# Kernel optimization log

Hardware: AMD Instinct MI355X
Metric: run time of the kernel (lower is better)

The kernel has to match this reference:

```python
import jax, jax.numpy as jnp
import numpy as np

D_MODEL = 1024
N_HEADS = 16
HEAD_DIM = D_MODEL // N_HEADS


def setup_inputs() -> dict:
    key = jax.random.key(0)
    ks = jax.random.split(key, 5)
    T, B = 2048, 2
    x = jax.random.normal(ks[0], (T, B, D_MODEL), dtype=jnp.float32)
    s = 1.0 / np.sqrt(D_MODEL)
    Wq = jax.random.normal(ks[1], (D_MODEL, D_MODEL), dtype=jnp.float32) * s
    Wk = jax.random.normal(ks[2], (D_MODEL, D_MODEL), dtype=jnp.float32) * s
    Wv = jax.random.normal(ks[3], (D_MODEL, D_MODEL), dtype=jnp.float32) * s
    Wo = jax.random.normal(ks[4], (D_MODEL, D_MODEL), dtype=jnp.float32) * s
    return {"x": x, "Wq": Wq, "Wk": Wk, "Wv": Wv, "Wo": Wo}


def reference(x, Wq, Wk, Wv, Wo):
    T, B, C = x.shape
    H, D = N_HEADS, HEAD_DIM

    def split_heads(t):
        # (T,B,C) -> (B,H,T,D), matching view+permute(1,2,0,3)
        return t.reshape(T, B, H, D).transpose(1, 2, 0, 3)

    q = split_heads(x @ Wq.T)
    k = split_heads(x @ Wk.T)
    v = split_heads(x @ Wv.T)

    scale = 1.0 / jnp.sqrt(jnp.asarray(D, dtype=x.dtype))
    scores = jnp.einsum('bhqd,bhkd->bhqk', q, k) * scale  # (B,H,T,T)
    causal = jnp.tril(jnp.ones((T, T), dtype=bool))
    scores = jnp.where(causal, scores, jnp.asarray(-jnp.inf, dtype=scores.dtype))
    probs = jax.nn.softmax(scores, axis=-1)
    ctx = jnp.einsum('bhqk,bhkd->bhqd', probs, v)  # (B,H,T,D)
    ctx = ctx.transpose(2, 0, 1, 3).reshape(T, B, C)
    return ctx @ Wo.T
```

## Files before the change

### kernel.cpp

```cpp
#include <hip/hip_runtime.h>
#include <hip/hip_bf16.h>

#define TT 2048
#define BB 2
#define CC 1024
#define HH 16
#define DD 64
#define MM (TT * BB)

typedef short bf16x8 __attribute__((ext_vector_type(8)));
typedef float f32x4  __attribute__((ext_vector_type(4)));

__device__ inline ushort f2b(float f) {
    union { float f; unsigned u; } v; v.f = f;
    unsigned r = v.u + 0x7FFFu + ((v.u >> 16) & 1u);
    return (ushort)(r >> 16);
}

__device__ inline unsigned pack_bf16(float a, float b) {
    __hip_bfloat162 h = __float22bfloat162_rn(make_float2(a, b));
    union { __hip_bfloat162 h; unsigned u; } c; c.h = h;
    return c.u;
}

__device__ inline void gload_lds16(const ushort* g, ushort* l) {
    __builtin_amdgcn_global_load_lds(
        (const __attribute__((address_space(1))) void*)g,
        (__attribute__((address_space(3))) void*)l, 16, 0, 0);
}

#define XQUADS (MM * CC / 4)
#define WQUADS (CC * CC / 4)
__global__ __launch_bounds__(256) void conv_all(const float* __restrict__ x,
                                                const float* __restrict__ Wq,
                                                const float* __restrict__ Wk,
                                                const float* __restrict__ Wv,
                                                const float* __restrict__ Wo,
                                                ushort* __restrict__ dst) {
    int idx = blockIdx.x * 256 + threadIdx.x;
    const float* src;
    int off;
    if (idx < XQUADS) {
        src = x; off = idx;
    } else {
        int wi = (idx - XQUADS) >> 18;
        off = (idx - XQUADS) & (WQUADS - 1);
        src = (wi == 0) ? Wq : (wi == 1) ? Wk : (wi == 2) ? Wv : Wo;
    }
    float4 v = ((const float4*)src)[off];
    ushort4 o = {f2b(v.x), f2b(v.y), f2b(v.z), f2b(v.w)};
    ((ushort4*)dst)[idx] = o;
}

__global__ __launch_bounds__(256) void gemm_qkv(const ushort* __restrict__ A,
                                                const ushort* __restrict__ B0,
                                                const ushort* __restrict__ B1,
                                                const ushort* __restrict__ B2,
                                                ushort* __restrict__ Oq,
                                                ushort* __restrict__ Ok,
                                                ushort* __restrict__ Ov) {
    __shared__ __align__(16) ushort As[128 * 32];
    __shared__ __align__(16) ushort Bs[128 * 32];

    const int tid = threadIdx.x;
    const int wave = tid >> 6, lane = tid & 63;
    const int quad = lane >> 4, l16 = lane & 15;
    const int wm = wave >> 1, wn = wave & 1;

    const int bm = blockIdx.x * 128;
    const int by = blockIdx.y;
    const int wsel = by >> 3;
    const ushort* Bp = (wsel == 0) ? B0 : (wsel == 1) ? B1 : B2;
    const int bn = (by & 7) * 128;

    const int srow = lane >> 2;
    const int scol = (lane & 3) * 8;

    f32x4 acc[4][4];
#pragma unroll
    for (int i = 0; i < 4; i++)
#pragma unroll
        for (int j = 0; j < 4; j++) acc[i][j] = (f32x4){0.f, 0.f, 0.f, 0.f};

    for (int k0 = 0; k0 < CC; k0 += 32) {
#pragma unroll
        for (int i = 0; i < 2; i++) {
            const int rbase = wave * 32 + i * 16;
            gload_lds16(A + (size_t)(bm + rbase + srow) * CC + k0 + scol,
                        As + rbase * 32);
            gload_lds16(Bp + (size_t)(bn + rbase + srow) * CC + k0 + scol,
                        Bs + rbase * 32);
        }
        __syncthreads();

        bf16x8 af[4], bf[4];
#pragma unroll
        for (int mi = 0; mi < 4; mi++)
            af[mi] = *(const bf16x8*)(As + (wm * 64 + mi * 16 + l16) * 32 + quad * 8);
#pragma unroll
        for (int ni = 0; ni < 4; ni++)
            bf[ni] = *(const bf16x8*)(Bs + (wn * 64 + ni * 16 + l16) * 32 + quad * 8);
#pragma unroll
        for (int mi = 0; mi < 4; mi++)
#pragma unroll
            for (int ni = 0; ni < 4; ni++)
                acc[mi][ni] = __builtin_amdgcn_mfma_f32_16x16x32_bf16(
                    af[mi], bf[ni], acc[mi][ni], 0, 0, 0);
        __syncthreads();
    }

#pragma unroll
    for (int mi = 0; mi < 4; mi++) {
#pragma unroll
        for (int r = 0; r < 4; r++) {
            const int m = bm + wm * 64 + mi * 16 + quad * 4 + r;
#pragma unroll
            for (int ni = 0; ni < 4; ni++) {
                const int colg = bn + wn * 64 + ni * 16 + l16;
                float v = acc[mi][ni][r];
                if (wsel == 0) v *= 0.18033688f;
                const int t = m >> 1, b = m & 1;
                const int h = colg >> 6, d = colg & 63;
                ushort* dst = (wsel == 0) ? Oq : (wsel == 1) ? Ok : Ov;
                dst[(((size_t)(b * HH + h)) * TT + t) * DD + d] = f2b(v);
            }
        }
    }
}

__global__ __launch_bounds__(256) void gemm_out(const ushort* __restrict__ A,
                                                const ushort* __restrict__ Bm,
                                                float* __restrict__ Of) {
    __shared__ __align__(16) ushort As[128 * 32];
    __shared__ __align__(16) ushort Bs[64 * 32];

    const int tid = threadIdx.x;
    const int wave = tid >> 6, lane = tid & 63;
    const int quad = lane >> 4, l16 = lane & 15;

    const int bm = blockIdx.x * 128;
    const int bn = blockIdx.y * 64;

    const int srow = lane >> 2;
    const int scol = (lane & 3) * 8;

    f32x4 acc[2][4];
#pragma unroll
    for (int i = 0; i < 2; i++)
#pragma unroll
        for (int j = 0; j < 4; j++) acc[i][j] = (f32x4){0.f, 0.f, 0.f, 0.f};

    for (int k0 = 0; k0 < CC; k0 += 32) {
#pragma unroll
        for (int i = 0; i < 2; i++) {
            const int rbase = wave * 32 + i * 16;
            gload_lds16(A + (size_t)(bm + rbase + srow) * CC + k0 + scol,
                        As + rbase * 32);
        }
        gload_lds16(Bm + (size_t)(bn + wave * 16 + srow) * CC + k0 + scol,
                    Bs + wave * 16 * 32);
        __syncthreads();

        bf16x8 af[2], bf[4];
#pragma unroll
        for (int mi = 0; mi < 2; mi++)
            af[mi] = *(const bf16x8*)(As + (wave * 32 + mi * 16 + l16) * 32 + quad * 8);
#pragma unroll
        for (int ni = 0; ni < 4; ni++)
            bf[ni] = *(const bf16x8*)(Bs + (ni * 16 + l16) * 32 + quad * 8);
#pragma unroll
        for (int mi = 0; mi < 2; mi++)
#pragma unroll
            for (int ni = 0; ni < 4; ni++)
                acc[mi][ni] = __builtin_amdgcn_mfma_f32_16x16x32_bf16(
                    af[mi], bf[ni], acc[mi][ni], 0, 0, 0);
        __syncthreads();
    }

#pragma unroll
    for (int mi = 0; mi < 2; mi++)
#pragma unroll
        for (int r = 0; r < 4; r++) {
            const int m = bm + wave * 32 + mi * 16 + quad * 4 + r;
#pragma unroll
            for (int ni = 0; ni < 4; ni++)
                Of[(size_t)m * CC + bn + ni * 16 + l16] = acc[mi][ni][r];
        }
}

__global__ __launch_bounds__(256) void prep_kv(const ushort* __restrict__ Kb,
                                               const ushort* __restrict__ Vb,
                                               ushort* __restrict__ Kf,
                                               ushort* __restrict__ Vf) {
    __shared__ __align__(16) ushort Ls[64 * 72];
    const int tile = blockIdx.x;
    const int bh   = blockIdx.y;
    const int t    = threadIdx.x;
    const size_t src = (size_t)bh * TT * DD + (size_t)tile * 64 * DD;
    const size_t dst = (size_t)bh * TT * DD + (size_t)tile * 4096;

#pragma unroll
    for (int i = 0; i < 2; i++) {
        int e = t + i * 256;
        int r = e >> 3, kc = (e & 7) * 8;
        *(uint4*)(Ls + r * 72 + kc) = *(const uint4*)(Kb + src + r * 64 + kc);
    }
    __syncthreads();
#pragma unroll
    for (int i = 0; i < 2; i++) {
        int o = t + i * 256;
        int c = o >> 8, nb = (o >> 6) & 3, lane = o & 63;
        int quad = lane >> 4, l16 = lane & 15;
        int j = nb * 16 + l16, k0 = c * 32 + quad * 8;
        *(uint4*)(Kf + dst + (size_t)o * 8) = *(const uint4*)(Ls + j * 72 + k0);
    }
    __syncthreads();

#pragma unroll
    for (int i = 0; i < 2; i++) {
        int e = t + i * 256;
        int r = e >> 3, kc = (e & 7) * 8;
        *(uint4*)(Ls + r * 72 + kc) = *(const uint4*)(Vb + src + r * 64 + kc);
    }
    __syncthreads();
#pragma unroll
    for (int i = 0; i < 2; i++) {
        int o = t + i * 256;
        int c = o >> 8, db = (o >> 6) & 3, lane = o & 63;
        int quad = lane >> 4, l16 = lane & 15;
        int d = db * 16 + l16;
        ushort tmp[8];
#pragma unroll
        for (int u = 0; u < 8; u++) {
            int jp = c * 32 + quad * 8 + u;
            int j = (jp & 3) * 16 + (jp >> 2);
            tmp[u] = Ls[j * 72 + d];
        }
        *(uint4*)(Vf + dst + (size_t)o * 8) = *(uint4*)tmp;
    }
}

template <bool DIAG>
__device__ __forceinline__ void attn_step(const bf16x8* qa, f32x4* O, float* l,
                                          const bf16x8* kf, const bf16x8* vf,
                                          ushort* P, int j0, int qbase,
                                          int quad, int l16) {
    f32x4 S[4];
#pragma unroll
    for (int nb = 0; nb < 4; nb++) S[nb] = (f32x4){0.f, 0.f, 0.f, 0.f};
#pragma unroll
    for (int c = 0; c < 2; c++)
#pragma unroll
        for (int nb = 0; nb < 4; nb++)
            S[nb] = __builtin_amdgcn_mfma_f32_16x16x32_bf16(qa[c], kf[c * 4 + nb],
                                                            S[nb], 0, 0, 0);

#pragma unroll
    for (int r = 0; r < 4; r++) {
        const int qg = qbase + quad * 4 + r;
        float p[4];
#pragma unroll
        for (int nb = 0; nb < 4; nb++) {
            float s = S[nb][r];
            if (DIAG) { if (j0 + nb * 16 + l16 > qg) s = -1e30f; }
            p[nb] = __builtin_amdgcn_exp2f(s);
        }
        l[r] += (p[0] + p[1]) + (p[2] + p[3]);
        uint2 w; w.x = pack_bf16(p[0], p[1]); w.y = pack_bf16(p[2], p[3]);
        *(uint2*)(P + (quad * 4 + r) * 72 + l16 * 4) = w;
    }

#pragma unroll
    for (int c = 0; c < 2; c++) {
        bf16x8 pa = *(const bf16x8*)(P + l16 * 72 + c * 32 + quad * 8);
#pragma unroll
        for (int db = 0; db < 4; db++)
            O[db] = __builtin_amdgcn_mfma_f32_16x16x32_bf16(pa, vf[c * 4 + db],
                                                            O[db], 0, 0, 0);
    }
}

__global__ __launch_bounds__(256, 2) void attn_mfma(const ushort* __restrict__ Qb,
                                                    const ushort* __restrict__ Kf,
                                                    const ushort* __restrict__ Vf,
                                                    ushort* __restrict__ ctx) {
    __shared__ __align__(16) ushort PsA[4 * 16 * 72];
    __shared__ __align__(16) ushort PsB[4 * 16 * 72];

    const int tid  = threadIdx.x;
    const int wave = tid >> 6;
    const int lane = tid & 63;
    const int quad = lane >> 4;
    const int l16  = lane & 15;

    const int p  = blockIdx.x;
    const int bh = blockIdx.y;
    const int qtA = p, qtB = (TT / 64 - 1) - p;
    const int q0A = qtA * 64 + wave * 16;
    const int q0B = qtB * 64 + wave * 16;

    const size_t baseQK = (size_t)bh * TT * DD;

    bf16x8 qaA[2], qaB[2];
    {
        const ushort* qp = Qb + baseQK + (size_t)(q0A + l16) * DD + quad * 8;
        qaA[0] = *(const bf16x8*)(qp);
        qaA[1] = *(const bf16x8*)(qp + 32);
        const ushort* qp2 = Qb + baseQK + (size_t)(q0B + l16) * DD + quad * 8;
        qaB[0] = *(const bf16x8*)(qp2);
        qaB[1] = *(const bf16x8*)(qp2 + 32);
    }

    f32x4 OA[4], OB[4];
#pragma unroll
    for (int i = 0; i < 4; i++) {
        OA[i] = (f32x4){0.f, 0.f, 0.f, 0.f};
        OB[i] = (f32x4){0.f, 0.f, 0.f, 0.f};
    }
    float lA[4] = {0.f, 0.f, 0.f, 0.f};
    float lB[4] = {0.f, 0.f, 0.f, 0.f};

    ushort* PA = PsA + wave * 16 * 72;
    ushort* PB = PsB + wave * 16 * 72;

    const ushort* Kfp = Kf + baseQK;
    const ushort* Vfp = Vf + baseQK;

    for (int kt = 0; kt <= qtB; kt++) {
        const int j0 = kt * 64;

        bf16x8 kf[8], vf[8];
#pragma unroll
        for (int i = 0; i < 8; i++) {
            kf[i] = *(const bf16x8*)(Kfp + (i << 9) + lane * 8);
            vf[i] = *(const bf16x8*)(Vfp + (i << 9) + lane * 8);
        }

        if (kt == qtB)
            attn_step<true >(qaB, OB, lB, kf, vf, PB, j0, q0B, quad, l16);
        else
            attn_step<false>(qaB, OB, lB, kf, vf, PB, j0, q0B, quad, l16);

        if (kt < qtA)
            attn_step<false>(qaA, OA, lA, kf, vf, PA, j0, q0A, quad, l16);
        else if (kt == qtA)
            attn_step<true >(qaA, OA, lA, kf, vf, PA, j0, q0A, quad, l16);

        Kfp += 4096;
        Vfp += 4096;
    }

    const int b = bh >> 4, h = bh & 15;
#pragma unroll
    for (int r = 0; r < 4; r++) {
        float la = lA[r], lb = lB[r];
        la += __shfl_xor(la, 1); la += __shfl_xor(la, 2);
        la += __shfl_xor(la, 4); la += __shfl_xor(la, 8);
        lb += __shfl_xor(lb, 1); lb += __shfl_xor(lb, 2);
        lb += __shfl_xor(lb, 4); lb += __shfl_xor(lb, 8);
        const float invA = 1.f / la;
        const float invB = 1.f / lb;
        const int tA = q0A + quad * 4 + r;
        const int tB = q0B + quad * 4 + r;
#pragma unroll
        for (int db = 0; db < 4; db++) {
            ctx[((size_t)tA * BB + b) * CC + h * DD + db * 16 + l16] =
                f2b(OA[db][r] * invA);
            ctx[((size_t)tB * BB + b) * CC + h * DD + db * 16 + l16] =
                f2b(OB[db][r] * invB);
        }
    }
}

extern "C" void kernel_launch(void* const* d_in, const int* in_sizes, int n_in,
                              void* d_out, int out_size, void* d_ws, size_t ws_size,
                              hipStream_t stream) {
    const float* x  = (const float*)d_in[0];
    const float* Wq = (const float*)d_in[1];
    const float* Wk = (const float*)d_in[2];
    const float* Wv = (const float*)d_in[3];
    const float* Wo = (const float*)d_in[4];
    float* out = (float*)d_out;

    ushort* xb  = (ushort*)d_ws;
    ushort* Wb  = xb + (size_t)MM * CC;
    ushort* Wqb = Wb;
    ushort* Wkb = Wb + (size_t)CC * CC;
    ushort* Wvb = Wb + 2 * (size_t)CC * CC;
    ushort* Wob = Wb + 3 * (size_t)CC * CC;
    ushort* Qb  = Wb + 4 * (size_t)CC * CC;
    ushort* Kb  = Qb + (size_t)MM * CC;
    ushort* Vb  = Kb + (size_t)MM * CC;
    ushort* Kf  = Vb + (size_t)MM * CC;
    ushort* Vf  = Kf + (size_t)MM * CC;
    ushort* Ctxb = Vf + (size_t)MM * CC;

    conv_all<<<dim3((XQUADS + 4 * WQUADS) / 256), 256, 0, stream>>>(
        x, Wq, Wk, Wv, Wo, xb);

    gemm_qkv<<<dim3(MM / 128, 24), 256, 0, stream>>>(
        xb, Wqb, Wkb, Wvb, Qb, Kb, Vb);

    prep_kv<<<dim3(TT / 64, BB * HH), 256, 0, stream>>>(Kb, Vb, Kf, Vf);

    attn_mfma<<<dim3(TT / 128, BB * HH), 256, 0, stream>>>(Qb, Kf, Vf, Ctxb);

    gemm_out<<<dim3(MM / 128, CC / 64), 256, 0, stream>>>(Ctxb, Wob, out);
}
```

Measured before the change: 177.8 us.

## Split paired causal query tiles into separate blocks with heavy-first ordering

```diff
diff --git a/kernel.cpp b/kernel.cpp
--- a/kernel.cpp
+++ b/kernel.cpp
@@ -242,18 +242,30 @@
 
 template <bool DIAG>
 __device__ __forceinline__ void attn_step(const bf16x8* qa, f32x4* O, float* l,
-                                          const bf16x8* kf, const bf16x8* vf,
+                                          const ushort* Kfp, const ushort* Vfp,
                                           ushort* P, int j0, int qbase,
-                                          int quad, int l16) {
+                                          int quad, int l16, int lane) {
+    bf16x8 kf[8];
+#pragma unroll
+    for (int i = 0; i < 8; i++)
+        kf[i] = *(const bf16x8*)(Kfp + (i << 9) + lane * 8);
+
     f32x4 S[4];
 #pragma unroll
     for (int nb = 0; nb < 4; nb++) S[nb] = (f32x4){0.f, 0.f, 0.f, 0.f};
+    __builtin_amdgcn_s_setprio(1);
 #pragma unroll
     for (int c = 0; c < 2; c++)
 #pragma unroll
         for (int nb = 0; nb < 4; nb++)
             S[nb] = __builtin_amdgcn_mfma_f32_16x16x32_bf16(qa[c], kf[c * 4 + nb],
                                                             S[nb], 0, 0, 0);
+    __builtin_amdgcn_s_setprio(0);
+
+    bf16x8 vf[8];
+#pragma unroll
+    for (int i = 0; i < 8; i++)
+        vf[i] = *(const bf16x8*)(Vfp + (i << 9) + lane * 8);
 
 #pragma unroll
     for (int r = 0; r < 4; r++) {
@@ -270,6 +282,7 @@
         *(uint2*)(P + (quad * 4 + r) * 72 + l16 * 4) = w;
     }
 
+    __builtin_amdgcn_s_setprio(1);
 #pragma unroll
     for (int c = 0; c < 2; c++) {
         bf16x8 pa = *(const bf16x8*)(P + l16 * 72 + c * 32 + quad * 8);
@@ -278,14 +291,14 @@
             O[db] = __builtin_amdgcn_mfma_f32_16x16x32_bf16(pa, vf[c * 4 + db],
                                                             O[db], 0, 0, 0);
     }
-}
-
-__global__ __launch_bounds__(256, 2) void attn_mfma(const ushort* __restrict__ Qb,
+    __builtin_amdgcn_s_setprio(0);
+}
+
+__global__ __launch_bounds__(256, 4) void attn_mfma(const ushort* __restrict__ Qb,
                                                     const ushort* __restrict__ Kf,
                                                     const ushort* __restrict__ Vf,
                                                     ushort* __restrict__ ctx) {
-    __shared__ __align__(16) ushort PsA[4 * 16 * 72];
-    __shared__ __align__(16) ushort PsB[4 * 16 * 72];
+    __shared__ __align__(16) ushort Ps[4 * 16 * 72];
 
     const int tid  = threadIdx.x;
     const int wave = tid >> 6;
@@ -293,81 +306,48 @@
     const int quad = lane >> 4;
     const int l16  = lane & 15;
 
-    const int p  = blockIdx.x;
+    const int qt = (TT / 64 - 1) - blockIdx.x;
     const int bh = blockIdx.y;
-    const int qtA = p, qtB = (TT / 64 - 1) - p;
-    const int q0A = qtA * 64 + wave * 16;
-    const int q0B = qtB * 64 + wave * 16;
+    const int q0 = qt * 64 + wave * 16;
 
     const size_t baseQK = (size_t)bh * TT * DD;
 
-    bf16x8 qaA[2], qaB[2];
+    bf16x8 qa[2];
     {
-        const ushort* qp = Qb + baseQK + (size_t)(q0A + l16) * DD + quad * 8;
-        qaA[0] = *(const bf16x8*)(qp);
-        qaA[1] = *(const bf16x8*)(qp + 32);
-        const ushort* qp2 = Qb + baseQK + (size_t)(q0B + l16) * DD + quad * 8;
-        qaB[0] = *(const bf16x8*)(qp2);
-        qaB[1] = *(const bf16x8*)(qp2 + 32);
-    }
-
-    f32x4 OA[4], OB[4];
-#pragma unroll
-    for (int i = 0; i < 4; i++) {
-        OA[i] = (f32x4){0.f, 0.f, 0.f, 0.f};
-        OB[i] = (f32x4){0.f, 0.f, 0.f, 0.f};
-    }
-    float lA[4] = {0.f, 0.f, 0.f, 0.f};
-    float lB[4] = {0.f, 0.f, 0.f, 0.f};
-
-    ushort* PA = PsA + wave * 16 * 72;
-    ushort* PB = PsB + wave * 16 * 72;
+        const ushort* qp = Qb + baseQK + (size_t)(q0 + l16) * DD + quad * 8;
+        qa[0] = *(const bf16x8*)(qp);
+        qa[1] = *(const bf16x8*)(qp + 32);
+    }
+
+    f32x4 O[4];
+#pragma unroll
+    for (int i = 0; i < 4; i++) O[i] = (f32x4){0.f, 0.f, 0.f, 0.f};
+    float l[4] = {0.f, 0.f, 0.f, 0.f};
+
+    ushort* P = Ps + wave * 16 * 72;
 
     const ushort* Kfp = Kf + baseQK;
     const ushort* Vfp = Vf + baseQK;
 
-    for (int kt = 0; kt <= qtB; kt++) {
-        const int j0 = kt * 64;
-
-        bf16x8 kf[8], vf[8];
-#pragma unroll
-        for (int i = 0; i < 8; i++) {
-            kf[i] = *(const bf16x8*)(Kfp + (i << 9) + lane * 8);
-            vf[i] = *(const bf16x8*)(Vfp + (i << 9) + lane * 8);
-        }
-
-        if (kt == qtB)
-            attn_step<true >(qaB, OB, lB, kf, vf, PB, j0, q0B, quad, l16);
-        else
-            attn_step<false>(qaB, OB, lB, kf, vf, PB, j0, q0B, quad, l16);
-
-        if (kt < qtA)
-            attn_step<false>(qaA, OA, lA, kf, vf, PA, j0, q0A, quad, l16);
-        else if (kt == qtA)
-            attn_step<true >(qaA, OA, lA, kf, vf, PA, j0, q0A, quad, l16);
-
+    for (int kt = 0; kt < qt; kt++) {
+        attn_step<false>(qa, O, l, Kfp, Vfp, P, kt * 64, q0, quad, l16, lane);
         Kfp += 4096;
         Vfp += 4096;
     }
+    attn_step<true>(qa, O, l, Kfp, Vfp, P, qt * 64, q0, quad, l16, lane);
 
     const int b = bh >> 4, h = bh & 15;
 #pragma unroll
     for (int r = 0; r < 4; r++) {
-        float la = lA[r], lb = lB[r];
+        float la = l[r];
         la += __shfl_xor(la, 1); la += __shfl_xor(la, 2);
         la += __shfl_xor(la, 4); la += __shfl_xor(la, 8);
-        lb += __shfl_xor(lb, 1); lb += __shfl_xor(lb, 2);
-        lb += __shfl_xor(lb, 4); lb += __shfl_xor(lb, 8);
-        const float invA = 1.f / la;
-        const float invB = 1.f / lb;
-        const int tA = q0A + quad * 4 + r;
-        const int tB = q0B + quad * 4 + r;
+        const float inv = 1.f / la;
+        const int tq = q0 + quad * 4 + r;
 #pragma unroll
         for (int db = 0; db < 4; db++) {
-            ctx[((size_t)tA * BB + b) * CC + h * DD + db * 16 + l16] =
-                f2b(OA[db][r] * invA);
-            ctx[((size_t)tB * BB + b) * CC + h * DD + db * 16 + l16] =
-                f2b(OB[db][r] * invB);
+            ctx[((size_t)tq * BB + b) * CC + h * DD + db * 16 + l16] =
+                f2b(O[db][r] * inv);
         }
     }
 }
@@ -403,7 +383,7 @@
 
     prep_kv<<<dim3(TT / 64, BB * HH), 256, 0, stream>>>(Kb, Vb, Kf, Vf);
 
-    attn_mfma<<<dim3(TT / 128, BB * HH), 256, 0, stream>>>(Qb, Kf, Vf, Ctxb);
+    attn_mfma<<<dim3(TT / 64, BB * HH), 256, 0, stream>>>(Qb, Kf, Vf, Ctxb);
 
     gemm_out<<<dim3(MM / 128, CC / 64), 256, 0, stream>>>(Ctxb, Wob, out);
 }
```

New measurement: 203.2 us. 14.3% more time.
